# Kernel optimization log

Hardware: AMD Instinct MI355X
Metric: run time of the kernel (lower is better)

The kernel has to match this reference:

```python
import jax, jax.numpy as jnp
import numpy as np

B, S, E = 4, 2048, 1024


def setup_inputs() -> dict:
    key = jax.random.key(0)
    ks = jax.random.split(key, 7)
    s = 1.0 / np.sqrt(E)  # torch Linear default init scale (uniform bound)
    inp = {
        "input": jax.random.normal(ks[0], (B, S, E), dtype=jnp.float32),
        "masked": 1,
        "W_q": jax.random.uniform(ks[1], (E, E), jnp.float32, -s, s),
        "b_q": jax.random.uniform(ks[2], (E,), jnp.float32, -s, s),
        "W_k": jax.random.uniform(ks[3], (E, E), jnp.float32, -s, s),
        "b_k": jax.random.uniform(ks[4], (E,), jnp.float32, -s, s),
        "W_v": jax.random.uniform(ks[5], (E, E), jnp.float32, -s, s),
        "b_v": jax.random.uniform(ks[6], (E,), jnp.float32, -s, s),
    }
    return inp


def reference(input, masked, W_q, b_q, W_k, b_k, W_v, b_v):
    # torch.nn.Linear: y = x @ W.T + b
    q = jnp.einsum("bse,fe->bsf", input, W_q) + b_q
    k = jnp.einsum("bse,fe->bsf", input, W_k) + b_k
    v = jnp.einsum("bse,fe->bsf", input, W_v) + b_v
    d = q.shape[-1]
    scores = jnp.einsum("bqd,bkd->bqk", q, k) / jnp.sqrt(jnp.float32(d))
    if masked:
        Sq = scores.shape[1]
        causal = jnp.tril(jnp.ones((Sq, Sq), dtype=bool))  # [S,S], broadcast over batch
        scores = jnp.where(causal, scores, -jnp.inf)
    attn = jax.nn.softmax(scores, axis=-1)
    return jnp.einsum("bqk,bkd->bqd", attn, v)
```

## Files before the change

kernel.cpp:

```cpp
#include <hip/hip_runtime.h>

typedef _Float16 f16;
typedef f16 f16x8 __attribute__((ext_vector_type(8)));
typedef f16 f16x4v __attribute__((ext_vector_type(4)));
typedef float f32x4 __attribute__((ext_vector_type(4)));

__device__ __forceinline__ void async_ld16(const void* g, void* l) {
    __builtin_amdgcn_global_load_lds(
        (const __attribute__((address_space(1))) unsigned int*)g,
        (__attribute__((address_space(3))) unsigned int*)l, 16, 0, 0);
}

template <int MODE>
__global__ __launch_bounds__((MODE == 0) ? 256 : 512) void gemm_bt(
    const f16* __restrict__ A, long strideAb, int lda,
    const f16* __restrict__ Bt, long strideBb, int ldb,
    const float* __restrict__ b_q, const float* __restrict__ b_k,
    const float* __restrict__ b_v, float* __restrict__ rowsum,
    void* __restrict__ C0, void* __restrict__ C1, void* __restrict__ C2,
    long strideCb, int K,
    const int* __restrict__ maskedp)
{
    constexpr int NT  = (MODE == 0) ? 256 : 512;
    constexpr int NI  = (MODE == 0) ? 4 : 2;
    constexpr int RND = (128 * 32) / (NT * 8);

    const int bx = blockIdx.x, bz = blockIdx.z;
    const int by = (MODE >= 2) ? (gridDim.y - 1 - blockIdx.y) : blockIdx.y;
    const int masked = maskedp ? *maskedp : 1;
    if (MODE == 2 && masked && bx > by) return;
    int kmax = K;
    if (MODE == 3 && masked) kmax = min(K, (by + 1) * 128);

    A  += (long)bz * strideAb;
    Bt += (long)bz * strideBb;

    __shared__ __align__(16) f16 smem[256 * 64];
    f16* sA = smem;
    f16* sB = smem + 128 * 64;

    const int tid  = threadIdx.x;
    const int wave = tid >> 6, lane = tid & 63;
    const int wrow = wave >> 1, wcol = wave & 1;
    const int quad = lane >> 4, l16 = lane & 15;
    const int mBase = by * 128, nBase = bx * 128;

    f32x4 acc[NI][4];
#pragma unroll
    for (int i = 0; i < NI; ++i)
#pragma unroll
        for (int j = 0; j < 4; ++j)
            acc[i][j] = (f32x4){0.f, 0.f, 0.f, 0.f};

    const f16* aP[RND];
    const f16* bP[RND];
#pragma unroll
    for (int r = 0; r < RND; ++r) {
        aP[r] = A  + (long)(mBase + ((r * NT + tid) >> 2)) * lda + ((tid * 8) & 31);
        bP[r] = Bt + (long)(nBase + ((r * NT + tid) >> 2)) * ldb + ((tid * 8) & 31);
    }
    const int ldsOff = wave * 512;

    const int nT = kmax >> 6;
    for (int kt = 0; kt < nT; ++kt) {
#pragma unroll
        for (int h = 0; h < 2; ++h)
#pragma unroll
            for (int r = 0; r < RND; ++r) {
                async_ld16(aP[r] + h * 32, &sA[h * 4096 + r * (NT * 8) + ldsOff]);
                async_ld16(bP[r] + h * 32, &sB[h * 4096 + r * (NT * 8) + ldsOff]);
            }
#pragma unroll
        for (int r = 0; r < RND; ++r) { aP[r] += 64; bP[r] += 64; }
        __syncthreads();

#pragma unroll
        for (int h = 0; h < 2; ++h) {
            f16x8 af[NI], bf[4];
#pragma unroll
            for (int i = 0; i < NI; ++i)
                af[i] = *(const f16x8*)&sA[h * 4096 + (wrow * (16 * NI) + i * 16 + l16) * 32 + quad * 8];
#pragma unroll
            for (int j = 0; j < 4; ++j)
                bf[j] = *(const f16x8*)&sB[h * 4096 + (wcol * 64 + j * 16 + l16) * 32 + quad * 8];
#pragma unroll
            for (int i = 0; i < NI; ++i)
#pragma unroll
                for (int j = 0; j < 4; ++j)
                    acc[i][j] = __builtin_amdgcn_mfma_f32_16x16x32_f16(af[i], bf[j], acc[i][j], 0, 0, 0);
        }
        __syncthreads();
    }

    if (MODE == 0) {
        const int seg = nBase >> 10;
        const float* bs = (seg == 0) ? b_q : (seg == 1) ? b_k : b_v;
        const int lcb = (nBase & 1023) + wcol * 64;
        float bvv[4];
#pragma unroll
        for (int j = 0; j < 4; ++j) bvv[j] = bs[lcb + j * 16 + l16];

        if (seg < 2) {
            f16* dst = (seg == 0) ? (f16*)C0 : (f16*)C1;
#pragma unroll
            for (int i = 0; i < 4; ++i)
#pragma unroll
                for (int j = 0; j < 4; ++j)
#pragma unroll
                    for (int r = 0; r < 4; ++r) {
                        const int row = mBase + wrow * 64 + i * 16 + quad * 4 + r;
                        dst[(long)row * 1024 + lcb + j * 16 + l16] = (f16)(acc[i][j][r] + bvv[j]);
                    }
        } else {
            const int b = mBase >> 11, s0 = mBase & 2047;
            f16* epiT = smem;
#pragma unroll
            for (int h = 0; h < 2; ++h) {
                if (wcol == h) {
#pragma unroll
                    for (int i = 0; i < 4; ++i)
#pragma unroll
                        for (int j = 0; j < 4; ++j) {
                            f16x4v pk;
#pragma unroll
                            for (int r = 0; r < 4; ++r)
                                pk[r] = (f16)(acc[i][j][r] + bvv[j]);
                            *(f16x4v*)&epiT[(j * 16 + l16) * 136 + wrow * 64 + i * 16 + quad * 4] = pk;
                        }
                }
                __syncthreads();
                const int er = tid >> 2;
                f16* dst = (f16*)C2 +
                    ((long)b * 1024 + (nBase & 1023) + h * 64 + er) * 2048 + s0;
#pragma unroll
                for (int cc = 0; cc < 4; ++cc) {
                    const int ch = (tid & 3) + cc * 4;
                    *(f16x8*)&dst[ch * 8] = *(const f16x8*)&epiT[er * 136 + ch * 8];
                }
                __syncthreads();
            }
        }
    } else if (MODE == 2) {
        f16* Crow = (f16*)C0 + (long)bz * strideCb;
        float* rsb = rowsum + bz * 2048;
#pragma unroll
        for (int i = 0; i < NI; ++i) {
            float rs[4] = {0.f, 0.f, 0.f, 0.f};
#pragma unroll
            for (int j = 0; j < 4; ++j)
#pragma unroll
                for (int r = 0; r < 4; ++r) {
                    const int row = mBase + wrow * 32 + i * 16 + quad * 4 + r;
                    const int col = nBase + wcol * 64 + j * 16 + l16;
                    float e = __expf(acc[i][j][r] * 0.03125f);
                    if (masked && col > row) e = 0.f;
                    const f16 hv = (f16)e;
                    Crow[(long)row * 2048 + col] = hv;
                    rs[r] += (float)hv;
                }
#pragma unroll
            for (int r = 0; r < 4; ++r) {
                float s = rs[r];
                s += __shfl_xor(s, 1);
                s += __shfl_xor(s, 2);
                s += __shfl_xor(s, 4);
                s += __shfl_xor(s, 8);
                if (l16 == 0) {
                    const int row = mBase + wrow * 32 + i * 16 + quad * 4 + r;
                    atomicAdd(&rsb[row], s);
                }
            }
        }
    } else {
        float* Crow = (float*)C0 + (long)bz * strideCb;
        const float* rsb = rowsum + bz * 2048;
#pragma unroll
        for (int i = 0; i < NI; ++i)
#pragma unroll
            for (int r = 0; r < 4; ++r) {
                const int row = mBase + wrow * 32 + i * 16 + quad * 4 + r;
                const float inv = 1.f / rsb[row];
#pragma unroll
                for (int j = 0; j < 4; ++j) {
                    const int col = nBase + wcol * 64 + j * 16 + l16;
                    Crow[(long)row * 1024 + col] = acc[i][j][r] * inv;
                }
            }
    }
}

__global__ void cvt_inp(const float* __restrict__ in, f16* __restrict__ out, int n4)
{
    const int i = blockIdx.x * blockDim.x + threadIdx.x;
    if (i >= n4) return;
    const float4 v = ((const float4*)in)[i];
    f16x4v o;
    o[0] = (f16)v.x; o[1] = (f16)v.y; o[2] = (f16)v.z; o[3] = (f16)v.w;
    ((f16x4v*)out)[i] = o;
}

__global__ void cvt_w3(const float* __restrict__ W0, const float* __restrict__ W1,
                       const float* __restrict__ W2, f16* __restrict__ out)
{
    const int bxx = blockIdx.x;
    const int which = bxx >> 10;
    const float* src = (which == 0) ? W0 : (which == 1) ? W1 : W2;
    const int i = (bxx & 1023) * 256 + threadIdx.x;
    const float4 v = ((const float4*)src)[i];
    f16x4v o;
    o[0] = (f16)v.x; o[1] = (f16)v.y; o[2] = (f16)v.z; o[3] = (f16)v.w;
    ((f16x4v*)(out + (long)which * 1024 * 1024))[i] = o;
}

extern "C" void kernel_launch(void* const* d_in, const int* in_sizes, int n_in,
                              void* d_out, int out_size, void* d_ws, size_t ws_size,
                              hipStream_t stream)
{
    const float* inp = (const float*)d_in[0];
    const int* masked = (const int*)d_in[1];
    const float* Wq = (const float*)d_in[2];
    const float* bq = (const float*)d_in[3];
    const float* Wk = (const float*)d_in[4];
    const float* bk = (const float*)d_in[5];
    const float* Wv = (const float*)d_in[6];
    const float* bv = (const float*)d_in[7];
    float* out = (float*)d_out;

    const int Bb = 4, S = 2048, E = 1024;
    const long nTok = (long)Bb * S;

    char* ws = (char*)d_ws;
    f16* inp16 = (f16*)ws;   ws += nTok * E * 2;
    f16* W3    = (f16*)ws;   ws += (long)3 * E * E * 2;
    f16* Q16   = (f16*)ws;   ws += nTok * E * 2;
    f16* K16   = (f16*)ws;   ws += nTok * E * 2;
    f16* Vt16  = (f16*)ws;   ws += nTok * E * 2;
    f16* P16   = (f16*)ws;   ws += (long)Bb * S * S * 2;
    float* rsum = (float*)ws; ws += nTok * 4;

    dim3 blk(256);

    hipMemsetAsync(rsum, 0, nTok * 4, stream);
    cvt_inp<<<(int)(nTok * E / 4 / 256), blk, 0, stream>>>(inp, inp16, (int)(nTok * E / 4));
    cvt_w3<<<3 * 1024, blk, 0, stream>>>(Wq, Wk, Wv, W3);

    gemm_bt<0><<<dim3(3 * E / 128, (int)(nTok / 128), 1), blk, 0, stream>>>(
        inp16, 0, E, W3, 0, E, bq, bk, bv, nullptr,
        Q16, K16, Vt16, 0, E, nullptr);

    gemm_bt<2><<<dim3(S / 128, S / 128, Bb), dim3(512), 0, stream>>>(
        Q16, (long)S * E, E, K16, (long)S * E, E, nullptr, nullptr, nullptr, rsum,
        P16, nullptr, nullptr, (long)S * S, E, masked);

    gemm_bt<3><<<dim3(E / 128, S / 128, Bb), dim3(512), 0, stream>>>(
        P16, (long)S * S, S, Vt16, (long)E * S, S, nullptr, nullptr, nullptr, rsum,
        out, nullptr, nullptr, (long)S * E, S, masked);
}
```

Before: 265.2 us.

## Replace QKV projection GEMM with 256x256-tile ping-pong pipelined kernel

Adds a dedicated QKV projection kernel using 256x256 output tiles with 512 threads, double-buffered async global-to-LDS loads interleaved with MFMA phases, s_setprio and a block-index swizzle for L2 locality. The larger tile raises arithmetic intensity and cuts global reloads of A and B compared with the previous 128x128 generic kernel. It uses 128KB of shared memory per block and hand-placed waitcnt and barriers, which makes the schedule fragile. The grid is 384 blocks, so load balance across CUs may be uneven.

```diff
diff --git a/kernel.cpp b/kernel.cpp
--- a/kernel.cpp
+++ b/kernel.cpp
@@ -9,6 +9,169 @@
     __builtin_amdgcn_global_load_lds(
         (const __attribute__((address_space(1))) unsigned int*)g,
         (__attribute__((address_space(3))) unsigned int*)l, 16, 0, 0);
+}
+
+__global__ __launch_bounds__(512, 2) void qkv256(
+    const f16* __restrict__ A, const f16* __restrict__ Bt,
+    const float* __restrict__ b_q, const float* __restrict__ b_k,
+    const float* __restrict__ b_v,
+    f16* __restrict__ Q16, f16* __restrict__ K16, f16* __restrict__ Vt16)
+{
+    constexpr int LDA = 1024;
+    int bid = blockIdx.x;
+    bid = (bid & 7) * 48 + (bid >> 3);
+    const int by = bid / 12, bx = bid - by * 12;
+    const int mBase = by * 256, nBase = bx * 256;
+
+    __shared__ __align__(16) f16 smem[65536];
+
+    const int tid = threadIdx.x;
+    const int wave = tid >> 6, lane = tid & 63;
+    const int wrow = wave >> 2, wcol = wave & 3;
+    const int quad = lane >> 4, l16 = lane & 15;
+
+    const int rowLane = tid >> 2;
+    const int cOff = ((tid & 3) ^ ((tid >> 3) & 3)) * 8;
+    const f16* pA  = A  + (long)(mBase + rowLane) * LDA + cOff;
+    const f16* pA1 = pA + 128 * LDA;
+    const f16* pB  = Bt + (long)(nBase + rowLane) * LDA + cOff;
+    const f16* pB1 = pB + 128 * LDA;
+    const int stgBase = wave * 1024;
+
+    const int swz  = (quad ^ ((l16 >> 1) & 3)) * 16;
+    const int aOff = (wrow * 128 + l16) * 64 + swz;
+    const int bOff = (wcol * 64 + l16) * 64 + swz;
+
+    f32x4 acc[8][4];
+#pragma unroll
+    for (int m = 0; m < 8; ++m)
+#pragma unroll
+        for (int n = 0; n < 4; ++n) acc[m][n] = (f32x4){0.f, 0.f, 0.f, 0.f};
+    f16x8 af[8], bf[4];
+
+#define STG(b, op, kh, P, P1, tOff) do {                                        \
+    char* d_ = (char*)smem + (b) * 65536 + (op) * 32768 + (kh) * 16384 + stgBase; \
+    async_ld16((P)  + (tOff) * 64 + (kh) * 32, d_);                             \
+    async_ld16((P1) + (tOff) * 64 + (kh) * 32, d_ + 8192);                      \
+} while (0)
+#define RD_A(b, kk) do {                                                        \
+    const char* s_ = (const char*)smem + (b) * 65536 + (kk) * 16384 + aOff;     \
+    _Pragma("unroll") for (int m_ = 0; m_ < 8; ++m_)                            \
+        af[m_] = *(const f16x8*)(s_ + m_ * 1024);                               \
+} while (0)
+#define RD_B2(b, kk, n0_) do {                                                  \
+    const char* s_ = (const char*)smem + (b) * 65536 + 32768 + (kk) * 16384 + bOff; \
+    bf[(n0_)]     = *(const f16x8*)(s_ + ((n0_)) * 1024);                       \
+    bf[(n0_) + 1] = *(const f16x8*)(s_ + ((n0_) + 1) * 1024);                   \
+} while (0)
+#define FENCE_MM(n0_) do {                                                      \
+    __builtin_amdgcn_s_barrier();                                               \
+    asm volatile("s_waitcnt lgkmcnt(0)" ::: "memory");                          \
+    __builtin_amdgcn_sched_barrier(0);                                          \
+    __builtin_amdgcn_s_setprio(1);                                              \
+    _Pragma("unroll") for (int m_ = 0; m_ < 8; ++m_) {                          \
+        acc[m_][(n0_)]     = __builtin_amdgcn_mfma_f32_16x16x32_f16(af[m_], bf[(n0_)],     acc[m_][(n0_)],     0, 0, 0); \
+        acc[m_][(n0_) + 1] = __builtin_amdgcn_mfma_f32_16x16x32_f16(af[m_], bf[(n0_) + 1], acc[m_][(n0_) + 1], 0, 0, 0); \
+    }                                                                           \
+    __builtin_amdgcn_s_setprio(0);                                              \
+} while (0)
+#define VMC(n) asm volatile("s_waitcnt vmcnt(" #n ")" ::: "memory")
+#define BAR __builtin_amdgcn_s_barrier()
+
+    STG(0, 0, 0, pA, pA1, 0); STG(0, 1, 0, pB, pB1, 0);
+    STG(0, 0, 1, pA, pA1, 0); STG(0, 1, 1, pB, pB1, 0);
+    STG(1, 0, 0, pA, pA1, 1); STG(1, 1, 0, pB, pB1, 1);
+    VMC(4);
+    BAR;
+
+#pragma unroll 1
+    for (int i = 0; i < 7; ++i) {
+        RD_A(0, 0); RD_B2(0, 0, 0); STG(1, 0, 1, pA, pA1, 1);
+        FENCE_MM(0); BAR;
+        RD_B2(0, 0, 2);             STG(1, 1, 1, pB, pB1, 1);
+        FENCE_MM(2); BAR;
+        RD_A(0, 1); RD_B2(0, 1, 0); STG(0, 0, 0, pA, pA1, 2);
+        FENCE_MM(0); BAR;
+        RD_B2(0, 1, 2);             STG(0, 1, 0, pB, pB1, 2);
+        FENCE_MM(2); VMC(4); BAR;
+        RD_A(1, 0); RD_B2(1, 0, 0); STG(0, 0, 1, pA, pA1, 2);
+        FENCE_MM(0); BAR;
+        RD_B2(1, 0, 2);             STG(0, 1, 1, pB, pB1, 2);
+        FENCE_MM(2); BAR;
+        RD_A(1, 1); RD_B2(1, 1, 0); STG(1, 0, 0, pA, pA1, 3);
+        FENCE_MM(0); BAR;
+        RD_B2(1, 1, 2);             STG(1, 1, 0, pB, pB1, 3);
+        FENCE_MM(2); VMC(4); BAR;
+        pA += 128; pA1 += 128; pB += 128; pB1 += 128;
+    }
+    RD_A(0, 0); RD_B2(0, 0, 0); STG(1, 0, 1, pA, pA1, 1);
+    FENCE_MM(0); BAR;
+    RD_B2(0, 0, 2);             STG(1, 1, 1, pB, pB1, 1);
+    FENCE_MM(2); BAR;
+    RD_A(0, 1); RD_B2(0, 1, 0);
+    FENCE_MM(0); BAR;
+    RD_B2(0, 1, 2);
+    FENCE_MM(2); VMC(0); BAR;
+    RD_A(1, 0); RD_B2(1, 0, 0);
+    FENCE_MM(0); BAR;
+    RD_B2(1, 0, 2);
+    FENCE_MM(2); BAR;
+    RD_A(1, 1); RD_B2(1, 1, 0);
+    FENCE_MM(0); BAR;
+    RD_B2(1, 1, 2);
+    FENCE_MM(2); BAR;
+
+    const int seg = nBase >> 10;
+    const float* bs = (seg == 0) ? b_q : (seg == 1) ? b_k : b_v;
+    const int lcb = (nBase & 1023) + wcol * 64;
+    float bvv[4];
+#pragma unroll
+    for (int n = 0; n < 4; ++n) bvv[n] = bs[lcb + n * 16 + l16];
+
+    if (seg < 2) {
+        f16* dst = (seg == 0) ? Q16 : K16;
+#pragma unroll
+        for (int m = 0; m < 8; ++m)
+#pragma unroll
+            for (int n = 0; n < 4; ++n)
+#pragma unroll
+                for (int r = 0; r < 4; ++r) {
+                    const int row = mBase + wrow * 128 + m * 16 + quad * 4 + r;
+                    dst[(long)row * 1024 + lcb + n * 16 + l16] =
+                        (f16)(acc[m][n][r] + bvv[n]);
+                }
+    } else {
+        const int b = mBase >> 11, s0 = mBase & 2047;
+        const int e0 = (nBase & 1023) + wcol * 64;
+        f16* epiW = smem + wave * (64 * 80);
+#pragma unroll
+        for (int sb = 0; sb < 2; ++sb) {
+#pragma unroll
+            for (int m4 = 0; m4 < 4; ++m4)
+#pragma unroll
+                for (int n = 0; n < 4; ++n) {
+                    f16x4v pk;
+#pragma unroll
+                    for (int r = 0; r < 4; ++r)
+                        pk[r] = (f16)(acc[sb * 4 + m4][n][r] + bvv[n]);
+                    *(f16x4v*)&epiW[(n * 16 + l16) * 80 + m4 * 16 + quad * 4] = pk;
+                }
+            asm volatile("s_waitcnt lgkmcnt(0)" ::: "memory");
+#pragma unroll
+            for (int it = 0; it < 8; ++it) {
+                const int e = it * 8 + (lane >> 3);
+                const f16x8 v = *(const f16x8*)&epiW[e * 80 + (lane & 7) * 8];
+                *(f16x8*)(Vt16 + ((long)b * 1024 + e0 + e) * 2048 + s0 +
+                          wrow * 128 + sb * 64 + (lane & 7) * 8) = v;
+            }
+        }
+    }
+#undef STG
+#undef RD_A
+#undef RD_B2
+#undef FENCE_MM
+#undef VMC
+#undef BAR
 }
 
 template <int MODE>
@@ -244,9 +407,8 @@
     cvt_inp<<<(int)(nTok * E / 4 / 256), blk, 0, stream>>>(inp, inp16, (int)(nTok * E / 4));
     cvt_w3<<<3 * 1024, blk, 0, stream>>>(Wq, Wk, Wv, W3);
 
-    gemm_bt<0><<<dim3(3 * E / 128, (int)(nTok / 128), 1), blk, 0, stream>>>(
-        inp16, 0, E, W3, 0, E, bq, bk, bv, nullptr,
-        Q16, K16, Vt16, 0, E, nullptr);
+    qkv256<<<dim3(32 * 12), dim3(512), 0, stream>>>(
+        inp16, W3, bq, bk, bv, Q16, K16, Vt16);
 
     gemm_bt<2><<<dim3(S / 128, S / 128, Bb), dim3(512), 0, stream>>>(
         Q16, (long)S * E, E, K16, (long)S * E, E, nullptr, nullptr, nullptr, rsum,
```

New measurement: 257.1 us. 3.0% less time.
